# Performance work log

Hardware: AMD Instinct MI355X
Metric: run time of the kernel (lower is better)

The kernel has to match this reference:

```python
import jax, jax.numpy as jnp
import numpy as np

N, C, D, H, W = 2, 16, 32, 128, 128
CLAMP_MIN, CLAMP_MAX = 1e-8, 1e8


def setup_inputs() -> dict:
    key = jax.random.key(0)
    k1, k2, k3 = jax.random.split(key, 3)
    pred = jax.random.uniform(k1, (N, C, D, H, W), dtype=jnp.float32)
    # target holds the discretized ordinal label, replicated across channel dim
    t = jax.random.randint(k2, (N, 1, D, H, W), 0, C, dtype=jnp.int32)
    target = jnp.broadcast_to(t, (N, C, D, H, W)).astype(jnp.int32)
    mask = jax.random.randint(k3, (N, 1, D, H, W), 0, 2, dtype=jnp.int32)
    return {"pred": pred, "target": target, "mask": mask}


def reference(pred, target, mask):
    n, c, d, h, w = pred.shape
    valid = (mask[:, 0] > 0).reshape(-1)              # [N*D*H*W]
    # channel-first flatten: matches pred.transpose(0,1) then boolean index
    p = jnp.moveaxis(pred, 1, 0).reshape(c, -1)       # [C, M]
    t = jnppos = jnp.moveaxis(target, 1, 0).reshape(c, -1)  # [C, M]
    K = jnp.arange(c, dtype=jnp.int32)[:, None]       # [C, 1]
    m0 = (K <= t) & valid[None, :]                    # ordinal bins below label
    m1 = (K > t) & valid[None, :]                     # ordinal bins above label
    log_p = jnp.log(jnp.clip(p, CLAMP_MIN, CLAMP_MAX))
    log_1mp = jnp.log(jnp.clip(1.0 - p, CLAMP_MIN, CLAMP_MAX))
    s = jnp.sum(jnp.where(m0, log_p, 0.0)) + jnp.sum(jnp.where(m1, log_1mp, 0.0))
    S = jnp.sum(valid).astype(pred.dtype)             # number of masked voxels
    return s / (-S)
```

## Files before the change

kernel.cpp:

```cpp
#include <hip/hip_runtime.h>


constexpr int    kC    = 16;
constexpr int    kDHW  = 32 * 128 * 128;
constexpr long   kM    = 2L * kDHW;
constexpr int    kBlock = 256;
constexpr int    kGrid  = (int)(kM / 4 / kBlock);

__global__ void zero_ws_kernel(unsigned long long* ws) {
    if (threadIdx.x == 0) {
        reinterpret_cast<double*>(ws)[0] = 0.0;
        ws[1] = 0ull;
    }
}

__global__ __launch_bounds__(kBlock)
void ordloss_kernel(const float* __restrict__ pred,
                    const int*   __restrict__ target,
                    const int*   __restrict__ mask,
                    double*      __restrict__ ws) {
    const int  tid  = blockIdx.x * blockDim.x + threadIdx.x;
    const long base = (long)tid * 4;
    const int  n    = (int)(base / kDHW);
    const int  sp   = (int)(base - (long)n * kDHW);

    const int4 mk = *reinterpret_cast<const int4*>(mask + base);
    const int4 tg = *reinterpret_cast<const int4*>(target + (size_t)n * kC * kDHW + sp);

    const float* pbase = pred + (size_t)n * kC * kDHW + sp;

    float acc0 = 0.f, acc1 = 0.f, acc2 = 0.f, acc3 = 0.f;
    const int t0 = tg.x, t1 = tg.y, t2 = tg.z, t3 = tg.w;

    #pragma unroll
    for (int c = 0; c < kC; ++c) {
        const float4 p = *reinterpret_cast<const float4*>(pbase + (size_t)c * kDHW);
        float x0 = (c <= t0) ? p.x : 1.0f - p.x;
        float x1 = (c <= t1) ? p.y : 1.0f - p.y;
        float x2 = (c <= t2) ? p.z : 1.0f - p.z;
        float x3 = (c <= t3) ? p.w : 1.0f - p.w;
        acc0 += __logf(fmaxf(x0, 1e-8f));
        acc1 += __logf(fmaxf(x1, 1e-8f));
        acc2 += __logf(fmaxf(x2, 1e-8f));
        acc3 += __logf(fmaxf(x3, 1e-8f));
    }

    float lsum = (mk.x > 0 ? acc0 : 0.f) + (mk.y > 0 ? acc1 : 0.f)
               + (mk.z > 0 ? acc2 : 0.f) + (mk.w > 0 ? acc3 : 0.f);
    int   lcnt = (mk.x > 0) + (mk.y > 0) + (mk.z > 0) + (mk.w > 0);

    #pragma unroll
    for (int off = 32; off > 0; off >>= 1) {
        lsum += __shfl_down(lsum, off);
        lcnt += __shfl_down(lcnt, off);
    }

    __shared__ float swave[kBlock / 64];
    __shared__ int   cwave[kBlock / 64];
    const int lane = threadIdx.x & 63;
    const int wid  = threadIdx.x >> 6;
    if (lane == 0) { swave[wid] = lsum; cwave[wid] = lcnt; }
    __syncthreads();
    if (threadIdx.x == 0) {
        float bs = swave[0] + swave[1] + swave[2] + swave[3];
        int   bc = cwave[0] + cwave[1] + cwave[2] + cwave[3];
        atomicAdd(ws, (double)bs);
        atomicAdd(reinterpret_cast<unsigned long long*>(ws) + 1,
                  (unsigned long long)bc);
    }
}

__global__ void finalize_kernel(const double* __restrict__ ws,
                                float* __restrict__ out) {
    if (threadIdx.x == 0) {
        const double s   = ws[0];
        const double cnt = (double)reinterpret_cast<const unsigned long long*>(ws)[1];
        out[0] = (float)(s / (-cnt));
    }
}

extern "C" void kernel_launch(void* const* d_in, const int* in_sizes, int n_in,
                              void* d_out, int out_size, void* d_ws, size_t ws_size,
                              hipStream_t stream) {
    const float* pred   = (const float*)d_in[0];
    const int*   target = (const int*)d_in[1];
    const int*   mask   = (const int*)d_in[2];
    double*      ws     = (double*)d_ws;
    float*       out    = (float*)d_out;

    zero_ws_kernel<<<1, 64, 0, stream>>>((unsigned long long*)ws);
    ordloss_kernel<<<kGrid, kBlock, 0, stream>>>(pred, target, mask, ws);
    finalize_kernel<<<1, 64, 0, stream>>>(ws, out);
}
```

Measured before the change: 156.2 us.

## Replace global atomics with per-block partials and a dedicated reduce kernel

```diff
diff --git a/kernel.cpp b/kernel.cpp
--- a/kernel.cpp
+++ b/kernel.cpp
@@ -1,44 +1,39 @@
 #include <hip/hip_runtime.h>
 
 
-constexpr int    kC    = 16;
-constexpr int    kDHW  = 32 * 128 * 128;
-constexpr long   kM    = 2L * kDHW;
-constexpr int    kBlock = 256;
-constexpr int    kGrid  = (int)(kM / 4 / kBlock);
-
-__global__ void zero_ws_kernel(unsigned long long* ws) {
-    if (threadIdx.x == 0) {
-        reinterpret_cast<double*>(ws)[0] = 0.0;
-        ws[1] = 0ull;
-    }
-}
+constexpr int  kC     = 16;
+constexpr int  kDHW   = 32 * 128 * 128;
+constexpr long kM     = 2L * kDHW;
+constexpr int  kBlock = 256;
+constexpr int  kVox   = 4;
+constexpr int  kGrid  = (int)(kM / kVox / kBlock);
 
 __global__ __launch_bounds__(kBlock)
-void ordloss_kernel(const float* __restrict__ pred,
-                    const int*   __restrict__ target,
-                    const int*   __restrict__ mask,
-                    double*      __restrict__ ws) {
-    const int  tid  = blockIdx.x * blockDim.x + threadIdx.x;
-    const long base = (long)tid * 4;
-    const int  n    = (int)(base / kDHW);
-    const int  sp   = (int)(base - (long)n * kDHW);
+void ordloss_main(const float* __restrict__ pred,
+                  const int*   __restrict__ target,
+                  const int*   __restrict__ mask,
+                  float*       __restrict__ bsum,
+                  int*         __restrict__ bcnt) {
+    const int  tid  = blockIdx.x * kBlock + threadIdx.x;
+    const long base = (long)tid * kVox;
+    const int  n    = (int)(base >> 19);
+    const int  sp   = (int)(base & (kDHW - 1));
 
+    const float* pb = pred + ((size_t)n << 23) + sp;
+    float4 p[kC];
+    #pragma unroll
+    for (int c = 0; c < kC; ++c)
+        p[c] = *reinterpret_cast<const float4*>(pb + ((size_t)c << 19));
     const int4 mk = *reinterpret_cast<const int4*>(mask + base);
-    const int4 tg = *reinterpret_cast<const int4*>(target + (size_t)n * kC * kDHW + sp);
-
-    const float* pbase = pred + (size_t)n * kC * kDHW + sp;
+    const int4 tg = *reinterpret_cast<const int4*>(target + ((size_t)n << 23) + sp);
 
     float acc0 = 0.f, acc1 = 0.f, acc2 = 0.f, acc3 = 0.f;
-    const int t0 = tg.x, t1 = tg.y, t2 = tg.z, t3 = tg.w;
-
     #pragma unroll
     for (int c = 0; c < kC; ++c) {
-        const float4 p = *reinterpret_cast<const float4*>(pbase + (size_t)c * kDHW);
-        float x0 = (c <= t0) ? p.x : 1.0f - p.x;
-        float x1 = (c <= t1) ? p.y : 1.0f - p.y;
-        float x2 = (c <= t2) ? p.z : 1.0f - p.z;
-        float x3 = (c <= t3) ? p.w : 1.0f - p.w;
+        float x0 = (c <= tg.x) ? p[c].x : 1.0f - p[c].x;
+        float x1 = (c <= tg.y) ? p[c].y : 1.0f - p[c].y;
+        float x2 = (c <= tg.z) ? p[c].z : 1.0f - p[c].z;
+        float x3 = (c <= tg.w) ? p[c].w : 1.0f - p[c].w;
         acc0 += __logf(fmaxf(x0, 1e-8f));
         acc1 += __logf(fmaxf(x1, 1e-8f));
         acc2 += __logf(fmaxf(x2, 1e-8f));
@@ -54,7 +49,6 @@
         lsum += __shfl_down(lsum, off);
         lcnt += __shfl_down(lcnt, off);
     }
-
     __shared__ float swave[kBlock / 64];
     __shared__ int   cwave[kBlock / 64];
     const int lane = threadIdx.x & 63;
@@ -62,20 +56,34 @@
     if (lane == 0) { swave[wid] = lsum; cwave[wid] = lcnt; }
     __syncthreads();
     if (threadIdx.x == 0) {
-        float bs = swave[0] + swave[1] + swave[2] + swave[3];
-        int   bc = cwave[0] + cwave[1] + cwave[2] + cwave[3];
-        atomicAdd(ws, (double)bs);
-        atomicAdd(reinterpret_cast<unsigned long long*>(ws) + 1,
-                  (unsigned long long)bc);
+        bsum[blockIdx.x] = swave[0] + swave[1] + swave[2] + swave[3];
+        bcnt[blockIdx.x] = cwave[0] + cwave[1] + cwave[2] + cwave[3];
     }
 }
 
-__global__ void finalize_kernel(const double* __restrict__ ws,
-                                float* __restrict__ out) {
+__global__ __launch_bounds__(kBlock)
+void ordloss_reduce(const float* __restrict__ bsum,
+                    const int*   __restrict__ bcnt,
+                    float*       __restrict__ out) {
+    const float4 s4 = *reinterpret_cast<const float4*>(bsum + threadIdx.x * 4);
+    const int4   c4 = *reinterpret_cast<const int4*>(bcnt + threadIdx.x * 4);
+    double s = (double)s4.x + s4.y + s4.z + s4.w;
+    long   c = (long)c4.x + c4.y + c4.z + c4.w;
+    #pragma unroll
+    for (int off = 32; off > 0; off >>= 1) {
+        s += __shfl_down(s, off);
+        c += __shfl_down(c, off);
+    }
+    __shared__ double sw[kBlock / 64];
+    __shared__ long   cw[kBlock / 64];
+    const int lane = threadIdx.x & 63;
+    const int wid  = threadIdx.x >> 6;
+    if (lane == 0) { sw[wid] = s; cw[wid] = c; }
+    __syncthreads();
     if (threadIdx.x == 0) {
-        const double s   = ws[0];
-        const double cnt = (double)reinterpret_cast<const unsigned long long*>(ws)[1];
-        out[0] = (float)(s / (-cnt));
+        double S = sw[0] + sw[1] + sw[2] + sw[3];
+        long   C = cw[0] + cw[1] + cw[2] + cw[3];
+        out[0] = (float)(S / (double)(-C));
     }
 }
 
@@ -85,10 +93,10 @@
     const float* pred   = (const float*)d_in[0];
     const int*   target = (const int*)d_in[1];
     const int*   mask   = (const int*)d_in[2];
-    double*      ws     = (double*)d_ws;
+    float*       bsum   = (float*)d_ws;
+    int*         bcnt   = (int*)((char*)d_ws + kGrid * sizeof(float));
     float*       out    = (float*)d_out;
 
-    zero_ws_kernel<<<1, 64, 0, stream>>>((unsigned long long*)ws);
-    ordloss_kernel<<<kGrid, kBlock, 0, stream>>>(pred, target, mask, ws);
-    finalize_kernel<<<1, 64, 0, stream>>>(ws, out);
+    ordloss_main<<<kGrid, kBlock, 0, stream>>>(pred, target, mask, bsum, bcnt);
+    ordloss_reduce<<<1, kBlock, 0, stream>>>(bsum, bcnt, out);
 }
```

Result: faster. 137.2 us (-12.1%).
